# Performance work log

Hardware: AMD Instinct MI355X
Metric: run time of the kernel (lower is better)

The kernel has to match this reference:

```python
import jax, jax.numpy as jnp
import numpy as np

N, n, m, k = 100000, 32, 16, 32
MU = 100.0  # bubble kernel scale (init arg mu)


def setup_inputs() -> dict:
    key = jax.random.key(0)
    ks = jax.random.split(key, 7)
    x = jax.random.normal(ks[0], (N,), dtype=jnp.float32)
    # torch.nn.Linear(N, n): weight [n, N], bias [n]
    encoder_w = jax.random.normal(ks[1], (n, N), dtype=jnp.float32) / np.float32(np.sqrt(N))
    encoder_b = jnp.zeros((n,), dtype=jnp.float32)
    # decoder parameter [n, N]
    decoder = jax.random.normal(ks[2], (n, N), dtype=jnp.float32) / np.float32(np.sqrt(n))
    # torch.nn.Linear(n, n*m): weight [n*m, n], bias [n*m]
    bw_w = jax.random.normal(ks[3], (n * m, n), dtype=jnp.float32) / np.float32(np.sqrt(n))
    bw_b = jnp.zeros((n * m,), dtype=jnp.float32)
    neighbour_distance = jax.random.uniform(ks[4], (N, k), dtype=jnp.float32)
    neighbour_id = jax.random.randint(ks[5], (N, k), 0, N)
    clustering_labels = jax.random.randint(ks[6], (N,), 0, m)
    return {
        "x": x,
        "encoder_w": encoder_w,
        "encoder_b": encoder_b,
        "decoder": decoder,
        "bw_w": bw_w,
        "bw_b": bw_b,
        "neighbour_distance": neighbour_distance,
        "neighbour_id": neighbour_id,
        "clustering_labels": clustering_labels,
    }


def reference(x, encoder_w, encoder_b, decoder, bw_w, bw_b,
              neighbour_distance, neighbour_id, clustering_labels):
    # encode: [N] -> [n]
    encoded = x @ encoder_w.T + encoder_b
    # per-basis, per-cluster bandwidths: sigmoid(Linear)/60 -> [n, m] -> expand to [n, N]
    bandwidths = jax.nn.sigmoid(encoded @ bw_w.T + bw_b) / 60.0
    w = bandwidths.reshape(n, m)[:, clustering_labels]  # [n, N]
    # bubble window: relu(1 - d^2 / (w*mu)^2) -> [n, N, k]
    window = jax.nn.relu(1.0 - neighbour_distance[None, :, :] ** 2
                         / (w[:, :, None] * MU) ** 2)
    # normalization over axis 1 (the N axis), faithful to the source's dim=1
    window = window / jnp.sum(window, axis=1, keepdims=True)
    # gather decoder rows at neighbours, weight, reduce over k: [n, N]
    convolved_basis = jnp.sum(decoder[:, neighbour_id] * window, axis=-1)
    # [n] @ [n, N] -> [N]
    return encoded @ convolved_basis
```

## Files before the change

kernel.cpp:

```cpp
#include <hip/hip_runtime.h>
#include <hip/hip_fp16.h>

#define N_PTS 100000
#define MU_F  100.0f

typedef unsigned int uint;
typedef _Float16 h2 __attribute__((ext_vector_type(2)));
typedef float f2 __attribute__((ext_vector_type(2)));

#define E_SCALE 16384.0f
#define E_SCALE_INV (1.0f / 16384.0f)

static __device__ inline h2 h2pack(float a, float b) {
    return __builtin_bit_cast(h2, __builtin_amdgcn_cvt_pkrtz(a, b));
}
static __device__ inline float fdot2f(h2 a, h2 b, float c) {
    return __builtin_amdgcn_fdot2(a, b, c, false);
}
static __device__ inline h2 h2fma(h2 a, h2 b, h2 c) {
#if __has_builtin(__builtin_elementwise_fma)
    return __builtin_elementwise_fma(a, b, c);
#else
    return a * b + c;
#endif
}
static __device__ inline h2 h2max(h2 a, h2 b) {
#if __has_builtin(__builtin_elementwise_max)
    return __builtin_elementwise_max(a, b);
#else
    h2 r;
    r.x = a.x > b.x ? a.x : b.x;
    r.y = a.y > b.y ? a.y : b.y;
    return r;
#endif
}
static __device__ inline f2 f2max(f2 a, f2 b) {
#if __has_builtin(__builtin_elementwise_max)
    return __builtin_elementwise_max(a, b);
#else
    f2 r;
    r.x = fmaxf(a.x, b.x);
    r.y = fmaxf(a.y, b.y);
    return r;
#endif
}

#define ENC_BLKS 256
#define TR_BLKS  1563
#define S_BLKS   1024
#define NPAIRS   (N_PTS / 2)
#define S_CH     ((NPAIRS + S_BLKS - 1) / S_BLKS)
#define M_BLKS   2048
#define M_CH     ((NPAIRS + M_BLKS - 1) / M_BLKS)

__global__ __launch_bounds__(256) void k_prep(const float* __restrict__ x,
                                              const float* __restrict__ encW,
                                              const float* __restrict__ encB,
                                              float* __restrict__ enc) {
    int b = blockIdx.x;
    int row = b & 31;
    int chunk = b >> 5;
    const int CH = N_PTS / 8;
    int base = chunk * CH;
    const float4* W4 = reinterpret_cast<const float4*>(encW + (size_t)row * N_PTS + base);
    const float4* x4 = reinterpret_cast<const float4*>(x + base);
    const int nv = CH / 4;
    float acc = 0.f;
    for (int idx = threadIdx.x; idx < nv; idx += 256) {
        float4 w = W4[idx];
        float4 xv = x4[idx];
        acc += w.x * xv.x + w.y * xv.y + w.z * xv.z + w.w * xv.w;
    }
    #pragma unroll
    for (int off = 32; off > 0; off >>= 1) acc += __shfl_down(acc, off);
    __shared__ float sred[4];
    int wid = threadIdx.x >> 6;
    if ((threadIdx.x & 63) == 0) sred[wid] = acc;
    __syncthreads();
    if (threadIdx.x == 0) {
        float s = sred[0] + sred[1] + sred[2] + sred[3];
        if (chunk == 0) s += encB[row];
        atomicAdd(enc + row, s);
    }
}

__device__ inline void build_invF(const float* __restrict__ encL,
                                  const float* __restrict__ bw_w,
                                  const float* __restrict__ bw_b,
                                  float* __restrict__ invF) {
    for (int r = threadIdx.x; r < 512; r += 256) {
        int i = r >> 4, c = r & 15;
        float z = bw_b[r];
        const float* wr = bw_w + r * 32;
        #pragma unroll
        for (int p = 0; p < 32; ++p) z = fmaf(encL[p], wr[p], z);
        float s = 1.f / (1.f + __expf(-z));
        float wmu = s * (MU_F / 60.0f);
        invF[c * 32 + i] = 1.f / (wmu * wmu);
    }
}

__global__ __launch_bounds__(256, 4) void k_S(const float* __restrict__ enc_g,
                                              const float* __restrict__ bw_w,
                                              const float* __restrict__ bw_b,
                                              const float* __restrict__ nd,
                                              const int* __restrict__ labels,
                                              float* __restrict__ S,
                                              float* __restrict__ S_part,
                                              const float* __restrict__ dec,
                                              __half* __restrict__ decT) {
    int b = blockIdx.x;
    if (b >= S_BLKS) {
        __shared__ float tile[32][65];
        int j0 = (b - S_BLKS) * 64;
        int col = threadIdx.x & 63;
        int r0 = threadIdx.x >> 6;
        #pragma unroll
        for (int it = 0; it < 8; ++it) {
            int row = it * 4 + r0;
            int j = j0 + col;
            float v = (j < N_PTS) ? dec[(size_t)row * N_PTS + j] : 0.f;
            tile[row][col] = v;
        }
        __syncthreads();
        #pragma unroll
        for (int it = 0; it < 4; ++it) {
            int idx = it * 256 + threadIdx.x;
            int j = idx >> 4;
            int p = idx & 15;
            int jj = j0 + j;
            if (jj < N_PTS) {
                __half2 h = __halves2half2(__float2half(tile[2 * p][j]),
                                           __float2half(tile[2 * p + 1][j]));
                *reinterpret_cast<__half2*>(decT + (size_t)jj * 32 + 2 * p) = h;
            }
        }
        return;
    }

    __shared__ float encL[32];
    __shared__ float invF[512];
    __shared__ float Sloc[1024];
    if (threadIdx.x < 32) encL[threadIdx.x] = enc_g[threadIdx.x];
    for (int t = threadIdx.x; t < 1024; t += 256) Sloc[t] = 0.f;
    __syncthreads();
    build_invF(encL, bw_w, bw_b, invF);
    __syncthreads();

    int lane = threadIdx.x & 63;
    int kk = lane & 31;
    int jh = lane >> 5;
    int w = threadIdx.x >> 6;
    int start = b * S_CH;
    int pend = min(start + S_CH, NPAIRS);
    int p = start + w;

    f2 acc2[16];
    #pragma unroll
    for (int t = 0; t < 16; ++t) { acc2[t].x = 0.f; acc2[t].y = 0.f; }

    if (p < pend) {
        auto ld4 = [&](int pbase, float* d, int* cc) {
            #pragma unroll
            for (int u = 0; u < 4; ++u) {
                int pc = pbase + 4 * u;
                int pcl = min(pc, NPAIRS - 1);
                int j = 2 * pcl + jh;
                float dv = __builtin_nontemporal_load(&nd[(size_t)j * 32 + kk]);
                cc[u] = labels[j];
                d[u] = (pc < pend) ? dv : 1.0e15f;
            }
        };
        float dA[4], dB[4]; int cA[4], cB[4];
        ld4(p, dA, cA);
        f2 onev; onev.x = 1.f; onev.y = 1.f;
        f2 zero2f; zero2f.x = 0.f; zero2f.y = 0.f;
        while (p < pend) {
            ld4(p + 16, dB, cB);
            __builtin_amdgcn_sched_barrier(0);
            f2 md[4];
            const float4* ivp[4];
            #pragma unroll
            for (int u = 0; u < 4; ++u) {
                float d2 = dA[u] * dA[u];
                md[u].x = -d2; md[u].y = -d2;
                ivp[u] = reinterpret_cast<const float4*>(&invF[cA[u] * 32]);
            }
            #pragma unroll
            for (int t4 = 0; t4 < 8; ++t4) {
                #pragma unroll
                for (int u = 0; u < 4; ++u) {
                    float4 iv = ivp[u][t4];
                    f2 i01; i01.x = iv.x; i01.y = iv.y;
                    f2 i23; i23.x = iv.z; i23.y = iv.w;
                    acc2[2 * t4]     += f2max(md[u] * i01 + onev, zero2f);
                    acc2[2 * t4 + 1] += f2max(md[u] * i23 + onev, zero2f);
                }
            }
            #pragma unroll
            for (int u = 0; u < 4; ++u) { dA[u] = dB[u]; cA[u] = cB[u]; }
            p += 16;
        }
    }
    #pragma unroll
    for (int t = 0; t < 16; ++t) {
        acc2[t].x += __shfl_xor(acc2[t].x, 32);
        acc2[t].y += __shfl_xor(acc2[t].y, 32);
    }
    if (jh == 0) {
        #pragma unroll
        for (int t = 0; t < 16; ++t) {
            atomicAdd(&Sloc[(2 * t) * 32 + kk], acc2[t].x);
            atomicAdd(&Sloc[(2 * t + 1) * 32 + kk], acc2[t].y);
        }
    }
    __syncthreads();
    if (S_part) {
        for (int t = threadIdx.x; t < 1024; t += 256)
            S_part[(size_t)b * 1024 + t] = Sloc[t];
    } else {
        for (int t = threadIdx.x; t < 1024; t += 256) {
            float v = Sloc[t];
            if (v != 0.f) atomicAdd(&S[t], v);
        }
    }
}

__global__ __launch_bounds__(1024) void k_S_reduce(const float* __restrict__ S_part,
                                                   float* __restrict__ S) {
    int g = blockIdx.x;
    int t = threadIdx.x;
    float s = 0.f;
    #pragma unroll
    for (int u = 0; u < 16; ++u)
        s += S_part[(size_t)(g * 16 + u) * 1024 + t];
    atomicAdd(&S[t], s);
}

__global__ __launch_bounds__(256, 4) void k_main(const float* __restrict__ enc_g,
                                                 const float* __restrict__ bw_w,
                                                 const float* __restrict__ bw_b,
                                                 const float* __restrict__ S_g,
                                                 const float* __restrict__ nd,
                                                 const int* __restrict__ nid,
                                                 const int* __restrict__ labels,
                                                 const __half* __restrict__ decT,
                                                 float* __restrict__ out) {
    __shared__ float encL[32];
    __shared__ float invF[512];
    __shared__ float ELf[1024];
    __shared__ h2 invHL[256];

    if (threadIdx.x < 32) encL[threadIdx.x] = enc_g[threadIdx.x];
    __syncthreads();
    build_invF(encL, bw_w, bw_b, invF);
    for (int t = threadIdx.x; t < 1024; t += 256)
        ELf[t] = encL[t >> 5] / S_g[t] * E_SCALE;
    __syncthreads();
    {
        int t = threadIdx.x;
        int c = t >> 4, q = (t >> 2) & 3, tt = t & 3;
        int i0 = q * 8 + 2 * tt;
        invHL[t] = h2pack(fminf(invF[c * 32 + i0], 6.0e4f),
                          fminf(invF[c * 32 + i0 + 1], 6.0e4f));
    }
    __syncthreads();

    int lane = threadIdx.x & 63;
    int R = lane >> 2;
    int q = lane & 3;

    h2 EhA[4], EhB[4];
    #pragma unroll
    for (int t = 0; t < 4; ++t) {
        int i0 = q * 8 + 2 * t;
        EhA[t] = h2pack(ELf[i0 * 32 + R], ELf[(i0 + 1) * 32 + R]);
        EhB[t] = h2pack(ELf[i0 * 32 + R + 16], ELf[(i0 + 1) * 32 + R + 16]);
    }
    const h2 zero2 = h2pack(0.f, 0.f);
    const h2 one2 = h2pack(1.f, 1.f);

    int w = threadIdx.x >> 6;
    int start = blockIdx.x * M_CH;
    int pend = min(start + M_CH, NPAIRS);
    int pa = start + w;
    const uint4* decQ = reinterpret_cast<const uint4*>(decT);
    if (pa >= pend) return;

    auto load_ldd = [&](int pc, int* id, float* dd, int& c0, int& c1) {
        pc = min(pc, NPAIRS - 1);
        int j0 = 2 * pc, j1 = j0 + 1;
        #pragma unroll
        for (int s = 0; s < 4; ++s) {
            size_t idx = (size_t)((s >> 1) ? j1 : j0) * 32 + (s & 1) * 16 + R;
            id[s] = __builtin_nontemporal_load(&nid[idx]);
            dd[s] = __builtin_nontemporal_load(&nd[idx]);
        }
        c0 = labels[j0];
        c1 = labels[j1];
    };
    auto load_rows = [&](const int* id, uint4* r) {
        #pragma unroll
        for (int s = 0; s < 4; ++s)
            r[s] = decQ[(size_t)id[s] * 4 + q];
    };
    auto load_ih = [&](int c0, int c1, h2* ih0, h2* ih1) {
        uint4 a = *reinterpret_cast<const uint4*>(&invHL[c0 * 16 + q * 4]);
        uint4 bq = *reinterpret_cast<const uint4*>(&invHL[c1 * 16 + q * 4]);
        ih0[0] = __builtin_bit_cast(h2, a.x);  ih0[1] = __builtin_bit_cast(h2, a.y);
        ih0[2] = __builtin_bit_cast(h2, a.z);  ih0[3] = __builtin_bit_cast(h2, a.w);
        ih1[0] = __builtin_bit_cast(h2, bq.x); ih1[1] = __builtin_bit_cast(h2, bq.y);
        ih1[2] = __builtin_bit_cast(h2, bq.z); ih1[3] = __builtin_bit_cast(h2, bq.w);
    };

    int ida[4], idb[4]; float dda[4], ddb[4];
    int ca0, ca1, cb0, cb1;
    uint4 ra[4], rb[4];
    h2 ihA0[4], ihA1[4];

    load_ldd(pa, ida, dda, ca0, ca1);
    load_ldd(pa + 4, idb, ddb, cb0, cb1);
    load_rows(ida, ra);
    load_ih(ca0, ca1, ihA0, ihA1);

    while (pa < pend) {
        load_rows(idb, rb);
        h2 ihB0[4], ihB1[4];
        load_ih(cb0, cb1, ihB0, ihB1);
        int idc[4]; float ddc[4]; int cc0, cc1;
        load_ldd(pa + 8, idc, ddc, cc0, cc1);
        __builtin_amdgcn_sched_barrier(0);

        float d20 = dda[0] * dda[0];
        float d21 = dda[1] * dda[1];
        float d22 = dda[2] * dda[2];
        float d23 = dda[3] * dda[3];
        h2 md0 = h2pack(-d20, -d20);
        h2 md1 = h2pack(-d21, -d21);
        h2 md2 = h2pack(-d22, -d22);
        h2 md3 = h2pack(-d23, -d23);

        float a0 = 0.f, a1 = 0.f, a2 = 0.f, a3 = 0.f;
        #pragma unroll
        for (int t = 0; t < 4; ++t) {
            uint dw0 = (t == 0) ? ra[0].x : (t == 1) ? ra[0].y : (t == 2) ? ra[0].z : ra[0].w;
            uint dw1 = (t == 0) ? ra[1].x : (t == 1) ? ra[1].y : (t == 2) ? ra[1].z : ra[1].w;
            uint dw2 = (t == 0) ? ra[2].x : (t == 1) ? ra[2].y : (t == 2) ? ra[2].z : ra[2].w;
            uint dw3 = (t == 0) ? ra[3].x : (t == 1) ? ra[3].y : (t == 2) ? ra[3].z : ra[3].w;
            {
                h2 wv = h2max(h2fma(md0, ihA0[t], one2), zero2);
                a0 = fdot2f(wv * EhA[t], __builtin_bit_cast(h2, dw0), a0);
            }
            {
                h2 wv = h2max(h2fma(md1, ihA0[t], one2), zero2);
                a1 = fdot2f(wv * EhB[t], __builtin_bit_cast(h2, dw1), a1);
            }
            {
                h2 wv = h2max(h2fma(md2, ihA1[t], one2), zero2);
                a2 = fdot2f(wv * EhA[t], __builtin_bit_cast(h2, dw2), a2);
            }
            {
                h2 wv = h2max(h2fma(md3, ihA1[t], one2), zero2);
                a3 = fdot2f(wv * EhB[t], __builtin_bit_cast(h2, dw3), a3);
            }
        }
        float u = a0 + a1;
        float v = a2 + a3;
        #pragma unroll
        for (int off = 32; off > 0; off >>= 1) {
            u += __shfl_xor(u, off);
            v += __shfl_xor(v, off);
        }
        if (lane == 0)  out[2 * pa]     = u * E_SCALE_INV;
        if (lane == 32) out[2 * pa + 1] = v * E_SCALE_INV;

        ca0 = cb0; ca1 = cb1; cb0 = cc0; cb1 = cc1;
        #pragma unroll
        for (int s = 0; s < 4; ++s) {
            dda[s] = ddb[s]; ddb[s] = ddc[s];
            ida[s] = idb[s]; idb[s] = idc[s];
            ra[s] = rb[s];
            ihA0[s] = ihB0[s]; ihA1[s] = ihB1[s];
        }
        pa += 4;
    }
}

extern "C" void kernel_launch(void* const* d_in, const int* in_sizes, int n_in,
                              void* d_out, int out_size, void* d_ws, size_t ws_size,
                              hipStream_t stream) {
    const float* x     = (const float*)d_in[0];
    const float* enc_w = (const float*)d_in[1];
    const float* enc_b = (const float*)d_in[2];
    const float* dec   = (const float*)d_in[3];
    const float* bw_w  = (const float*)d_in[4];
    const float* bw_b  = (const float*)d_in[5];
    const float* nd    = (const float*)d_in[6];
    const int*   nid   = (const int*)d_in[7];
    const int*   labels= (const int*)d_in[8];
    float* out = (float*)d_out;

    char* ws = (char*)d_ws;
    float* enc    = (float*)(ws + 0);
    float* S      = (float*)(ws + 128);
    __half* decT  = (__half*)(ws + 532480);
    bool use_part = ws_size >= 11126784ull;
    float* S_part = use_part ? (float*)(ws + 6932480) : nullptr;

    (void)hipMemsetAsync(d_ws, 0, 4224, stream);
    k_prep<<<dim3(ENC_BLKS), dim3(256), 0, stream>>>(x, enc_w, enc_b, enc);
    k_S<<<dim3(S_BLKS + TR_BLKS), dim3(256), 0, stream>>>(
        enc, bw_w, bw_b, nd, labels, S, S_part, dec, decT);
    if (use_part)
        k_S_reduce<<<dim3(64), dim3(1024), 0, stream>>>(S_part, S);
    k_main<<<dim3(M_BLKS), dim3(256), 0, stream>>>(enc, bw_w, bw_b, S, nd, nid,
                                                   labels, decT, out);
}
```

Baseline: 203.8 us.

## Precompute bandwidth and scaled-encoding tables in tiny kernels instead of per block

Moves the per-block recomputation of the sigmoid bandwidth table (512 32-wide dot products) and the E/S scaling table out of k_S and k_main into two single-block kernels, k_tab and k_elf, that write them to workspace. The large kernels now only copy the ready tables into shared memory or registers, which shortens their prologues and trims shared memory. Occupancy hints are raised from 4 to 8 blocks per CU. The cost is two extra serial kernel launches on the critical path.

```diff
diff --git a/kernel.cpp b/kernel.cpp
--- a/kernel.cpp
+++ b/kernel.cpp
@@ -84,25 +84,44 @@
     }
 }
 
-__device__ inline void build_invF(const float* __restrict__ encL,
-                                  const float* __restrict__ bw_w,
-                                  const float* __restrict__ bw_b,
-                                  float* __restrict__ invF) {
+__global__ __launch_bounds__(256) void k_tab(const float* __restrict__ enc_g,
+                                             const float* __restrict__ bw_w,
+                                             const float* __restrict__ bw_b,
+                                             float* __restrict__ invFG,
+                                             h2* __restrict__ invHLG) {
+    __shared__ float encL[32];
+    __shared__ float invF[512];
+    if (threadIdx.x < 32) encL[threadIdx.x] = enc_g[threadIdx.x];
+    __syncthreads();
     for (int r = threadIdx.x; r < 512; r += 256) {
         int i = r >> 4, c = r & 15;
+        const float4* wr4 = reinterpret_cast<const float4*>(bw_w + (size_t)r * 32);
         float z = bw_b[r];
-        const float* wr = bw_w + r * 32;
-        #pragma unroll
-        for (int p = 0; p < 32; ++p) z = fmaf(encL[p], wr[p], z);
+        #pragma unroll
+        for (int p4 = 0; p4 < 8; ++p4) {
+            float4 wv = wr4[p4];
+            z = fmaf(encL[4 * p4 + 0], wv.x, z);
+            z = fmaf(encL[4 * p4 + 1], wv.y, z);
+            z = fmaf(encL[4 * p4 + 2], wv.z, z);
+            z = fmaf(encL[4 * p4 + 3], wv.w, z);
+        }
         float s = 1.f / (1.f + __expf(-z));
         float wmu = s * (MU_F / 60.0f);
-        invF[c * 32 + i] = 1.f / (wmu * wmu);
-    }
-}
-
-__global__ __launch_bounds__(256, 4) void k_S(const float* __restrict__ enc_g,
-                                              const float* __restrict__ bw_w,
-                                              const float* __restrict__ bw_b,
+        float iv = 1.f / (wmu * wmu);
+        invF[c * 32 + i] = iv;
+        invFG[c * 32 + i] = iv;
+    }
+    __syncthreads();
+    {
+        int t = threadIdx.x;
+        int c = t >> 4, q = (t >> 2) & 3, tt = t & 3;
+        int i0 = q * 8 + 2 * tt;
+        invHLG[t] = h2pack(fminf(invF[c * 32 + i0], 6.0e4f),
+                           fminf(invF[c * 32 + i0 + 1], 6.0e4f));
+    }
+}
+
+__global__ __launch_bounds__(256, 8) void k_S(const float* __restrict__ invFG,
                                               const float* __restrict__ nd,
                                               const int* __restrict__ labels,
                                               float* __restrict__ S,
@@ -138,13 +157,12 @@
         return;
     }
 
-    __shared__ float encL[32];
     __shared__ float invF[512];
     __shared__ float Sloc[1024];
-    if (threadIdx.x < 32) encL[threadIdx.x] = enc_g[threadIdx.x];
+    if (threadIdx.x < 128)
+        reinterpret_cast<float4*>(invF)[threadIdx.x] =
+            reinterpret_cast<const float4*>(invFG)[threadIdx.x];
     for (int t = threadIdx.x; t < 1024; t += 256) Sloc[t] = 0.f;
-    __syncthreads();
-    build_invF(encL, bw_w, bw_b, invF);
     __syncthreads();
 
     int lane = threadIdx.x & 63;
@@ -237,33 +255,39 @@
     atomicAdd(&S[t], s);
 }
 
-__global__ __launch_bounds__(256, 4) void k_main(const float* __restrict__ enc_g,
-                                                 const float* __restrict__ bw_w,
-                                                 const float* __restrict__ bw_b,
-                                                 const float* __restrict__ S_g,
+__global__ __launch_bounds__(256) void k_elf(const float* __restrict__ enc_g,
+                                             const float* __restrict__ S_g,
+                                             h2* __restrict__ EhG_A,
+                                             h2* __restrict__ EhG_B) {
+    __shared__ float encL[32];
+    __shared__ float ELf[1024];
+    if (threadIdx.x < 32) encL[threadIdx.x] = enc_g[threadIdx.x];
+    __syncthreads();
+    for (int t = threadIdx.x; t < 1024; t += 256)
+        ELf[t] = encL[t >> 5] / S_g[t] * E_SCALE;
+    __syncthreads();
+    {
+        int t = threadIdx.x;
+        int lane = t >> 2, tt = t & 3;
+        int R = lane >> 2, q = lane & 3;
+        int i0 = q * 8 + 2 * tt;
+        EhG_A[t] = h2pack(ELf[i0 * 32 + R],      ELf[(i0 + 1) * 32 + R]);
+        EhG_B[t] = h2pack(ELf[i0 * 32 + R + 16], ELf[(i0 + 1) * 32 + R + 16]);
+    }
+}
+
+__global__ __launch_bounds__(256, 8) void k_main(const h2* __restrict__ invHLG,
+                                                 const h2* __restrict__ EhG_A,
+                                                 const h2* __restrict__ EhG_B,
                                                  const float* __restrict__ nd,
                                                  const int* __restrict__ nid,
                                                  const int* __restrict__ labels,
                                                  const __half* __restrict__ decT,
                                                  float* __restrict__ out) {
-    __shared__ float encL[32];
-    __shared__ float invF[512];
-    __shared__ float ELf[1024];
     __shared__ h2 invHL[256];
-
-    if (threadIdx.x < 32) encL[threadIdx.x] = enc_g[threadIdx.x];
-    __syncthreads();
-    build_invF(encL, bw_w, bw_b, invF);
-    for (int t = threadIdx.x; t < 1024; t += 256)
-        ELf[t] = encL[t >> 5] / S_g[t] * E_SCALE;
-    __syncthreads();
-    {
-        int t = threadIdx.x;
-        int c = t >> 4, q = (t >> 2) & 3, tt = t & 3;
-        int i0 = q * 8 + 2 * tt;
-        invHL[t] = h2pack(fminf(invF[c * 32 + i0], 6.0e4f),
-                          fminf(invF[c * 32 + i0 + 1], 6.0e4f));
-    }
+    if (threadIdx.x < 64)
+        reinterpret_cast<uint4*>(invHL)[threadIdx.x] =
+            reinterpret_cast<const uint4*>(invHLG)[threadIdx.x];
     __syncthreads();
 
     int lane = threadIdx.x & 63;
@@ -271,11 +295,13 @@
     int q = lane & 3;
 
     h2 EhA[4], EhB[4];
-    #pragma unroll
-    for (int t = 0; t < 4; ++t) {
-        int i0 = q * 8 + 2 * t;
-        EhA[t] = h2pack(ELf[i0 * 32 + R], ELf[(i0 + 1) * 32 + R]);
-        EhB[t] = h2pack(ELf[i0 * 32 + R + 16], ELf[(i0 + 1) * 32 + R + 16]);
+    {
+        uint4 a = reinterpret_cast<const uint4*>(EhG_A)[lane];
+        uint4 bq = reinterpret_cast<const uint4*>(EhG_B)[lane];
+        EhA[0] = __builtin_bit_cast(h2, a.x);  EhA[1] = __builtin_bit_cast(h2, a.y);
+        EhA[2] = __builtin_bit_cast(h2, a.z);  EhA[3] = __builtin_bit_cast(h2, a.w);
+        EhB[0] = __builtin_bit_cast(h2, bq.x); EhB[1] = __builtin_bit_cast(h2, bq.y);
+        EhB[2] = __builtin_bit_cast(h2, bq.z); EhB[3] = __builtin_bit_cast(h2, bq.w);
     }
     const h2 zero2 = h2pack(0.f, 0.f);
     const h2 one2 = h2pack(1.f, 1.f);
@@ -403,16 +429,22 @@
     char* ws = (char*)d_ws;
     float* enc    = (float*)(ws + 0);
     float* S      = (float*)(ws + 128);
+    float* invFG  = (float*)(ws + 4224);
+    h2*    invHLG = (h2*)(ws + 6272);
+    h2*    EhG_A  = (h2*)(ws + 7296);
+    h2*    EhG_B  = (h2*)(ws + 8320);
     __half* decT  = (__half*)(ws + 532480);
     bool use_part = ws_size >= 11126784ull;
     float* S_part = use_part ? (float*)(ws + 6932480) : nullptr;
 
     (void)hipMemsetAsync(d_ws, 0, 4224, stream);
     k_prep<<<dim3(ENC_BLKS), dim3(256), 0, stream>>>(x, enc_w, enc_b, enc);
+    k_tab<<<dim3(1), dim3(256), 0, stream>>>(enc, bw_w, bw_b, invFG, invHLG);
     k_S<<<dim3(S_BLKS + TR_BLKS), dim3(256), 0, stream>>>(
-        enc, bw_w, bw_b, nd, labels, S, S_part, dec, decT);
+        invFG, nd, labels, S, S_part, dec, decT);
     if (use_part)
         k_S_reduce<<<dim3(64), dim3(1024), 0, stream>>>(S_part, S);
-    k_main<<<dim3(M_BLKS), dim3(256), 0, stream>>>(enc, bw_w, bw_b, S, nd, nid,
-                                                   labels, decT, out);
-}
+    k_elf<<<dim3(1), dim3(256), 0, stream>>>(enc, S, EhG_A, EhG_B);
+    k_main<<<dim3(M_BLKS), dim3(256), 0, stream>>>(invHLG, EhG_A, EhG_B,
+                                                   nd, nid, labels, decT, out);
+}
```

New measurement: 259.9 us. 27.5% more time.
